# Kernel tuning notes

Measured on AMD Instinct MI355X. Metric: run time of the kernel, lower is better.

The kernel has to match this reference:

```python
import jax, jax.numpy as jnp
import numpy as np

DIM = 512
NUM_HEADS = 16
HEAD_DIM = DIM // NUM_HEADS
HIDDEN = int(DIM * 4.0)
EPS = 1e-5


def layer_norm(x, gamma, beta):
    mu = jnp.mean(x, axis=-1, keepdims=True)
    var = jnp.mean(jnp.square(x - mu), axis=-1, keepdims=True)
    return (x - mu) * jax.lax.rsqrt(var + EPS) * gamma + beta


def setup_inputs() -> dict:
    key = jax.random.key(0)
    ks = jax.random.split(key, 8)
    B, L, C = 32, 3136, DIM
    x = jax.random.normal(ks[0], (B, L, C), dtype=jnp.float32)
    norm1_g = jnp.ones((C,), jnp.float32)
    norm1_b = jnp.zeros((C,), jnp.float32)
    # spatial (per-head) mixing weight: (num_heads, head_dim, head_dim)
    w_spatial = jax.random.normal(ks[1], (NUM_HEADS, HEAD_DIM, HEAD_DIM), jnp.float32) * (1.0 / np.sqrt(HEAD_DIM))
    norm2_g = jnp.ones((C,), jnp.float32)
    norm2_b = jnp.zeros((C,), jnp.float32)
    w1 = jax.random.normal(ks[2], (C, HIDDEN), jnp.float32) * (1.0 / np.sqrt(C))
    b1 = jnp.zeros((HIDDEN,), jnp.float32)
    w2 = jax.random.normal(ks[3], (HIDDEN, C), jnp.float32) * (1.0 / np.sqrt(HIDDEN))
    b2 = jnp.zeros((C,), jnp.float32)
    return {"x": x, "norm1_g": norm1_g, "norm1_b": norm1_b, "w_spatial": w_spatial,
            "norm2_g": norm2_g, "norm2_b": norm2_b, "w1": w1, "b1": b1, "w2": w2, "b2": b2}


def reference(x, norm1_g, norm1_b, w_spatial, norm2_g, norm2_b, w1, b1, w2, b2):
    B, L, C = x.shape
    shortcut = x
    h = layer_norm(x, norm1_g, norm1_b)
    # window partition -> per-head channel-sub-dim linear (shared across windows/positions)
    # mathematically equivalent to applying the per-head matmul at every token
    h = h.reshape(B, L, NUM_HEADS, HEAD_DIM)
    h = jnp.einsum('blhd,hde->blhe', h, w_spatial)
    h = h.reshape(B, L, C)
    x = shortcut + h
    # channel MLP: Linear -> GELU(tanh) -> Linear
    y = layer_norm(x, norm2_g, norm2_b)
    y = jax.nn.gelu(y @ w1 + b1, approximate=True)
    y = y @ w2 + b2
    return x + y
```

## Files before the change

### kernel.cpp

```cpp
#include <hip/hip_runtime.h>
#include <hip/hip_bf16.h>


typedef __bf16 bf16x8 __attribute__((ext_vector_type(8)));
typedef float f32x4 __attribute__((ext_vector_type(4)));

constexpr int CDIM = 512;
constexpr int HID = 2048;
constexpr int MROWS = 32 * 3136;
constexpr float LN_EPS = 1e-5f;

static __device__ __forceinline__ float gelu_tanh(float x) {
  const float u = 0.7978845608028654f * fmaf(0.044715f * x * x, x, x);
  const float e = __expf(2.0f * u);
  return 0.5f * x * (2.0f - 2.0f / (e + 1.0f));
}

static __device__ __forceinline__ void load_lds16(const void* g, void* l) {
  __builtin_amdgcn_global_load_lds((__attribute__((address_space(1))) void*)g,
                                   (__attribute__((address_space(3))) void*)l,
                                   16, 0, 0);
}

template <int KD, int ND>
__global__ __launch_bounds__(256) void cvt_pack(const float* __restrict__ src,
                                                __hip_bfloat16* __restrict__ dst) {
  constexpr int NKT = KD / 32;
  const int o = blockIdx.x * 256 + threadIdx.x;
  const int l = o & 63;
  const int gt = o >> 6;
  const int t = gt & (NKT - 1), g = gt / NKT;
  const int n = g * 16 + (l & 15);
  const int k0 = t * 32 + (l >> 4) * 8;
  __hip_bfloat16 v[8];
#pragma unroll
  for (int j = 0; j < 8; ++j)
    v[j] = __float2bfloat16(src[(size_t)(k0 + j) * ND + n]);
  *(uint4*)(dst + (size_t)o * 8) = *(const uint4*)v;
}

__global__ __launch_bounds__(256) void fused_pre(
    const float* __restrict__ x, const float* __restrict__ g1,
    const float* __restrict__ b1, const float* __restrict__ wsp,
    const float* __restrict__ g2, const float* __restrict__ b2,
    float* __restrict__ x2out, __hip_bfloat16* __restrict__ yout) {
  __shared__ float lnbuf[2][CDIM];
  __shared__ float red[16];

  const int t = threadIdx.x;
  const int lane = t & 63;
  const int w = t >> 6;
  const int c0 = 2 * t;
  const int hd = c0 >> 5, e0 = c0 & 31;

  float wc0[32], wc1[32];
#pragma unroll
  for (int d = 0; d < 32; ++d) {
    const float2 wv = *(const float2*)&wsp[(hd * 32 + d) * 32 + e0];
    wc0[d] = wv.x;
    wc1[d] = wv.y;
  }
  const float2 g1v = *(const float2*)&g1[c0];
  const float2 b1v = *(const float2*)&b1[c0];
  const float2 g2v = *(const float2*)&g2[c0];
  const float2 b2v = *(const float2*)&b2[c0];

  for (int rp = blockIdx.x; rp < MROWS / 2; rp += gridDim.x) {
    const size_t ra = (size_t)rp * 2, rb = ra + 1;
    const float2 xa = *(const float2*)&x[ra * CDIM + c0];
    const float2 xb = *(const float2*)&x[rb * CDIM + c0];

    float sa = xa.x + xa.y, qa = xa.x * xa.x + xa.y * xa.y;
    float sb = xb.x + xb.y, qb = xb.x * xb.x + xb.y * xb.y;
#pragma unroll
    for (int off = 32; off; off >>= 1) {
      sa += __shfl_down(sa, off);
      qa += __shfl_down(qa, off);
      sb += __shfl_down(sb, off);
      qb += __shfl_down(qb, off);
    }
    if (lane == 0) {
      red[w * 4 + 0] = sa;
      red[w * 4 + 1] = qa;
      red[w * 4 + 2] = sb;
      red[w * 4 + 3] = qb;
    }
    __syncthreads();
    sa = red[0] + red[4] + red[8] + red[12];
    qa = red[1] + red[5] + red[9] + red[13];
    sb = red[2] + red[6] + red[10] + red[14];
    qb = red[3] + red[7] + red[11] + red[15];
    float mua = sa * (1.0f / CDIM), mub = sb * (1.0f / CDIM);
    float rsa = rsqrtf(qa * (1.0f / CDIM) - mua * mua + LN_EPS);
    float rsb = rsqrtf(qb * (1.0f / CDIM) - mub * mub + LN_EPS);
    lnbuf[0][c0] = (xa.x - mua) * rsa * g1v.x + b1v.x;
    lnbuf[0][c0 + 1] = (xa.y - mua) * rsa * g1v.y + b1v.y;
    lnbuf[1][c0] = (xb.x - mub) * rsb * g1v.x + b1v.x;
    lnbuf[1][c0 + 1] = (xb.y - mub) * rsb * g1v.y + b1v.y;
    __syncthreads();

    float ha0 = 0.f, ha1 = 0.f, hb0 = 0.f, hb1 = 0.f;
#pragma unroll
    for (int d = 0; d < 32; ++d) {
      const float la = lnbuf[0][hd * 32 + d];
      const float lb = lnbuf[1][hd * 32 + d];
      ha0 = fmaf(la, wc0[d], ha0);
      ha1 = fmaf(la, wc1[d], ha1);
      hb0 = fmaf(lb, wc0[d], hb0);
      hb1 = fmaf(lb, wc1[d], hb1);
    }
    const float a0 = xa.x + ha0, a1 = xa.y + ha1;
    const float b0 = xb.x + hb0, b1r = xb.y + hb1;
    float2 av;
    av.x = a0;
    av.y = a1;
    *(float2*)&x2out[ra * CDIM + c0] = av;
    av.x = b0;
    av.y = b1r;
    *(float2*)&x2out[rb * CDIM + c0] = av;

    sa = a0 + a1;
    qa = a0 * a0 + a1 * a1;
    sb = b0 + b1r;
    qb = b0 * b0 + b1r * b1r;
#pragma unroll
    for (int off = 32; off; off >>= 1) {
      sa += __shfl_down(sa, off);
      qa += __shfl_down(qa, off);
      sb += __shfl_down(sb, off);
      qb += __shfl_down(qb, off);
    }
    if (lane == 0) {
      red[w * 4 + 0] = sa;
      red[w * 4 + 1] = qa;
      red[w * 4 + 2] = sb;
      red[w * 4 + 3] = qb;
    }
    __syncthreads();
    sa = red[0] + red[4] + red[8] + red[12];
    qa = red[1] + red[5] + red[9] + red[13];
    sb = red[2] + red[6] + red[10] + red[14];
    qb = red[3] + red[7] + red[11] + red[15];
    mua = sa * (1.0f / CDIM);
    mub = sb * (1.0f / CDIM);
    rsa = rsqrtf(qa * (1.0f / CDIM) - mua * mua + LN_EPS);
    rsb = rsqrtf(qb * (1.0f / CDIM) - mub * mub + LN_EPS);
    __hip_bfloat162 yv;
    yv.x = __float2bfloat16((a0 - mua) * rsa * g2v.x + b2v.x);
    yv.y = __float2bfloat16((a1 - mua) * rsa * g2v.y + b2v.y);
    *(__hip_bfloat162*)&yout[ra * CDIM + c0] = yv;
    yv.x = __float2bfloat16((b0 - mub) * rsb * g2v.x + b2v.x);
    yv.y = __float2bfloat16((b1r - mub) * rsb * g2v.y + b2v.y);
    *(__hip_bfloat162*)&yout[rb * CDIM + c0] = yv;
    __syncthreads();
  }
}

template <int K, int N, bool GELU>
__global__ __launch_bounds__(256, 3) void gemmbs(
    const __hip_bfloat16* __restrict__ A, const char* __restrict__ Bp,
    const float* __restrict__ bias, __hip_bfloat16* __restrict__ zout,
    float* __restrict__ fout) {
  constexpr int NT = N / 128;
  constexpr int NKT = K / 32;
  __shared__ __attribute__((aligned(16))) char smem[32768];

  const int tid = threadIdx.x;
  const int lane = tid & 63;
  const int w = tid >> 6;
  const int wr = w >> 1, wc = w & 1;

  const int cpx = gridDim.x >> 3;
  const int bid = (blockIdx.x & 7) * cpx + (blockIdx.x >> 3);
  const int tm = bid / NT, tn = bid - tm * NT;
  const size_t am0 = (size_t)tm * 128;
  const int bn0 = tn * 128;

  const int r0 = tid >> 2, q0 = tid & 3;
  const __hip_bfloat16* aP0 = A + (am0 + r0) * K + q0 * 8;
  const __hip_bfloat16* aP1 = aP0 + (size_t)64 * K;
  const int wb = w * 1024;

  const int fr = lane & 15;
  const int kb = (lane >> 4) * 16;
  const int abase = (wr * 64 + fr) * 64 + kb;

  const char* bBase = Bp + ((size_t)(tn * 8 + wc * 4) * NKT) * 1024 + lane * 16;

#define STAGE_A(so, kt)                                       \
  do {                                                        \
    load_lds16(aP0 + (kt) * 32, smem + (so) + wb);            \
    load_lds16(aP1 + (kt) * 32, smem + (so) + 4096 + wb);     \
  } while (0)

  f32x4 acc[4][4] = {};
  bf16x8 bf[4], bfn[4];

  STAGE_A(0, 0);
#pragma unroll
  for (int n = 0; n < 4; ++n)
    bf[n] = *(const bf16x8*)(bBase + ((size_t)n * NKT) * 1024);
  __syncthreads();

  for (int t = 0; t < NKT; ++t) {
    const int d = (t & 1) * 8192, dn = 8192 - d;
    if (t + 1 < NKT) {
      STAGE_A(dn, t + 1);
#pragma unroll
      for (int n = 0; n < 4; ++n)
        bfn[n] = *(const bf16x8*)(bBase + ((size_t)n * NKT + t + 1) * 1024);
    }

    bf16x8 af[4];
#pragma unroll
    for (int m = 0; m < 4; ++m)
      af[m] = *(const bf16x8*)(smem + d + abase + m * 1024);
#pragma unroll
    for (int m = 0; m < 4; ++m)
#pragma unroll
      for (int n = 0; n < 4; ++n)
        acc[m][n] = __builtin_amdgcn_mfma_f32_16x16x32_bf16(af[m], bf[n],
                                                            acc[m][n], 0, 0, 0);
    if (t + 1 < NKT) {
#pragma unroll
      for (int n = 0; n < 4; ++n) bf[n] = bfn[n];
    }
    __syncthreads();
  }
#undef STAGE_A

  const int cr = (lane >> 4) * 4;
  const int cc = lane & 15;
  char* smb = smem;

  if constexpr (GELU) {
    __hip_bfloat16* ot = (__hip_bfloat16*)smb;
#pragma unroll
    for (int n = 0; n < 4; ++n) {
      const int col = wc * 64 + n * 16 + cc;
      const float bv = bias[bn0 + col];
#pragma unroll
      for (int m = 0; m < 4; ++m) {
        const int row = wr * 64 + m * 16 + cr;
#pragma unroll
        for (int j = 0; j < 4; ++j)
          ot[(row + j) * 128 + col] =
              __float2bfloat16(gelu_tanh(acc[m][n][j] + bv));
      }
    }
    __syncthreads();
#pragma unroll
    for (int it = 0; it < 8; ++it) {
      const int seg = it * 256 + tid;
      const int row = seg >> 4, cs = seg & 15;
      const uint4 v = *(const uint4*)(smb + seg * 16);
      *(uint4*)&zout[(am0 + row) * N + bn0 + cs * 8] = v;
    }
  } else {
    float* ot = (float*)smb;
#pragma unroll
    for (int p = 0; p < 2; ++p) {
      if (p) __syncthreads();
      if (wr == p) {
#pragma unroll
        for (int n = 0; n < 4; ++n) {
          const int col = wc * 64 + n * 16 + cc;
          const float bv = bias[bn0 + col];
#pragma unroll
          for (int m = 0; m < 4; ++m) {
            const int rl = m * 16 + cr;
#pragma unroll
            for (int j = 0; j < 4; ++j)
              ot[(rl + j) * 128 + col] = acc[m][n][j] + bv;
          }
        }
      }
      __syncthreads();
#pragma unroll
      for (int it = 0; it < 8; ++it) {
        const int seg = it * 256 + tid;
        const int row = seg >> 5, cs = seg & 31;
        const float4 lv = *(const float4*)(smb + seg * 16);
        float* gp = &fout[(am0 + p * 64 + row) * N + bn0 + cs * 4];
        float4 o = *(const float4*)gp;
        o.x += lv.x;
        o.y += lv.y;
        o.z += lv.z;
        o.w += lv.w;
        *(float4*)gp = o;
      }
    }
  }
}

extern "C" void kernel_launch(void* const* d_in, const int* in_sizes, int n_in,
                              void* d_out, int out_size, void* d_ws,
                              size_t ws_size, hipStream_t stream) {
  const float* x = (const float*)d_in[0];
  const float* n1g = (const float*)d_in[1];
  const float* n1b = (const float*)d_in[2];
  const float* wsp = (const float*)d_in[3];
  const float* n2g = (const float*)d_in[4];
  const float* n2b = (const float*)d_in[5];
  const float* w1 = (const float*)d_in[6];
  const float* b1 = (const float*)d_in[7];
  const float* w2 = (const float*)d_in[8];
  const float* b2 = (const float*)d_in[9];
  float* out = (float*)d_out;

  __hip_bfloat16* ybuf = (__hip_bfloat16*)d_ws;
  __hip_bfloat16* zbuf = ybuf + (size_t)MROWS * CDIM;
  __hip_bfloat16* w1p = zbuf + (size_t)MROWS * HID;
  __hip_bfloat16* w2p = w1p + (size_t)CDIM * HID;

  cvt_pack<CDIM, HID><<<512, 256, 0, stream>>>(w1, w1p);
  cvt_pack<HID, CDIM><<<512, 256, 0, stream>>>(w2, w2p);
  fused_pre<<<2048, 256, 0, stream>>>(x, n1g, n1b, wsp, n2g, n2b, out, ybuf);
  gemmbs<CDIM, HID, true><<<(MROWS / 128) * (HID / 128), 256, 0, stream>>>(
      ybuf, (const char*)w1p, b1, zbuf, nullptr);
  gemmbs<HID, CDIM, false><<<(MROWS / 128) * (CDIM / 128), 256, 0, stream>>>(
      zbuf, (const char*)w2p, b2, nullptr, out);
}
```

Before: 880.6 us.

## Switch GEMMs from 16x16x32 to 32x32x16 bf16 MFMA tiles

Replaces the 4x4 grid of 16x16x32 MFMA accumulators per warp with a 2x2 grid of 32x32x16 MFMA accumulators. The packed B-weight layout, the A fragment LDS addressing and the epilogue row/column mapping are changed to match. The larger instruction is meant to raise operand reuse per MFMA and cut LDS fragment reads. The risk is LDS bank conflicts from the new A access pattern and a different epilogue store pattern.

```diff
diff --git a/kernel.cpp b/kernel.cpp
--- a/kernel.cpp
+++ b/kernel.cpp
@@ -3,7 +3,7 @@
 
 
 typedef __bf16 bf16x8 __attribute__((ext_vector_type(8)));
-typedef float f32x4 __attribute__((ext_vector_type(4)));
+typedef float f32x16 __attribute__((ext_vector_type(16)));
 
 constexpr int CDIM = 512;
 constexpr int HID = 2048;
@@ -23,15 +23,15 @@
 }
 
 template <int KD, int ND>
-__global__ __launch_bounds__(256) void cvt_pack(const float* __restrict__ src,
-                                                __hip_bfloat16* __restrict__ dst) {
-  constexpr int NKT = KD / 32;
+__global__ __launch_bounds__(256) void cvt_pack32(
+    const float* __restrict__ src, __hip_bfloat16* __restrict__ dst) {
+  constexpr int NKT2 = KD / 16;
   const int o = blockIdx.x * 256 + threadIdx.x;
   const int l = o & 63;
   const int gt = o >> 6;
-  const int t = gt & (NKT - 1), g = gt / NKT;
-  const int n = g * 16 + (l & 15);
-  const int k0 = t * 32 + (l >> 4) * 8;
+  const int t = gt & (NKT2 - 1), g = gt / NKT2;
+  const int n = g * 32 + (l & 31);
+  const int k0 = t * 16 + (l >> 5) * 8;
   __hip_bfloat16 v[8];
 #pragma unroll
   for (int j = 0; j < 8; ++j)
@@ -157,12 +157,13 @@
 }
 
 template <int K, int N, bool GELU>
-__global__ __launch_bounds__(256, 3) void gemmbs(
+__global__ __launch_bounds__(256, 3) void gemm32(
     const __hip_bfloat16* __restrict__ A, const char* __restrict__ Bp,
     const float* __restrict__ bias, __hip_bfloat16* __restrict__ zout,
     float* __restrict__ fout) {
   constexpr int NT = N / 128;
-  constexpr int NKT = K / 32;
+  constexpr int NKT2 = K / 16;
+  constexpr int NST = K / 32;
   __shared__ __attribute__((aligned(16))) char smem[32768];
 
   const int tid = threadIdx.x;
@@ -181,11 +182,12 @@
   const __hip_bfloat16* aP1 = aP0 + (size_t)64 * K;
   const int wb = w * 1024;
 
-  const int fr = lane & 15;
-  const int kb = (lane >> 4) * 16;
-  const int abase = (wr * 64 + fr) * 64 + kb;
-
-  const char* bBase = Bp + ((size_t)(tn * 8 + wc * 4) * NKT) * 1024 + lane * 16;
+  const int arow = (lane & 31);
+  const int akb = (lane >> 5) * 16;
+  const int abase = (wr * 64 + arow) * 64 + akb;
+
+  const char* bBase =
+      Bp + ((size_t)(tn * 4 + wc * 2) * NKT2) * 1024 + lane * 16;
 
 #define STAGE_A(so, kt)                                       \
   do {                                                        \
@@ -193,60 +195,72 @@
     load_lds16(aP1 + (kt) * 32, smem + (so) + 4096 + wb);     \
   } while (0)
 
-  f32x4 acc[4][4] = {};
-  bf16x8 bf[4], bfn[4];
+  f32x16 acc[2][2] = {};
+  bf16x8 bf[2][2], bfn[2][2], af[2][2];
 
   STAGE_A(0, 0);
 #pragma unroll
-  for (int n = 0; n < 4; ++n)
-    bf[n] = *(const bf16x8*)(bBase + ((size_t)n * NKT) * 1024);
+  for (int ni = 0; ni < 2; ++ni)
+#pragma unroll
+    for (int kh = 0; kh < 2; ++kh)
+      bf[ni][kh] = *(const bf16x8*)(bBase + ((size_t)ni * NKT2 + kh) * 1024);
   __syncthreads();
 
-  for (int t = 0; t < NKT; ++t) {
+  for (int t = 0; t < NST; ++t) {
     const int d = (t & 1) * 8192, dn = 8192 - d;
-    if (t + 1 < NKT) {
+    if (t + 1 < NST) {
       STAGE_A(dn, t + 1);
 #pragma unroll
-      for (int n = 0; n < 4; ++n)
-        bfn[n] = *(const bf16x8*)(bBase + ((size_t)n * NKT + t + 1) * 1024);
-    }
-
-    bf16x8 af[4];
-#pragma unroll
-    for (int m = 0; m < 4; ++m)
-      af[m] = *(const bf16x8*)(smem + d + abase + m * 1024);
-#pragma unroll
-    for (int m = 0; m < 4; ++m)
-#pragma unroll
-      for (int n = 0; n < 4; ++n)
-        acc[m][n] = __builtin_amdgcn_mfma_f32_16x16x32_bf16(af[m], bf[n],
-                                                            acc[m][n], 0, 0, 0);
-    if (t + 1 < NKT) {
-#pragma unroll
-      for (int n = 0; n < 4; ++n) bf[n] = bfn[n];
+      for (int ni = 0; ni < 2; ++ni)
+#pragma unroll
+        for (int kh = 0; kh < 2; ++kh)
+          bfn[ni][kh] = *(const bf16x8*)(bBase +
+                                         ((size_t)ni * NKT2 + 2 * (t + 1) + kh) *
+                                             1024);
+    }
+
+#pragma unroll
+    for (int mi = 0; mi < 2; ++mi)
+#pragma unroll
+      for (int kh = 0; kh < 2; ++kh)
+        af[mi][kh] =
+            *(const bf16x8*)(smem + d + abase + mi * 2048 + kh * 32);
+#pragma unroll
+    for (int kh = 0; kh < 2; ++kh)
+#pragma unroll
+      for (int mi = 0; mi < 2; ++mi)
+#pragma unroll
+        for (int ni = 0; ni < 2; ++ni)
+          acc[mi][ni] = __builtin_amdgcn_mfma_f32_32x32x16_bf16(
+              af[mi][kh], bf[ni][kh], acc[mi][ni], 0, 0, 0);
+    if (t + 1 < NST) {
+#pragma unroll
+      for (int ni = 0; ni < 2; ++ni)
+#pragma unroll
+        for (int kh = 0; kh < 2; ++kh) bf[ni][kh] = bfn[ni][kh];
     }
     __syncthreads();
   }
 #undef STAGE_A
 
-  const int cr = (lane >> 4) * 4;
-  const int cc = lane & 15;
+  const int ccol = lane & 31;
+  const int rbase = 4 * (lane >> 5);
   char* smb = smem;
 
   if constexpr (GELU) {
     __hip_bfloat16* ot = (__hip_bfloat16*)smb;
 #pragma unroll
-    for (int n = 0; n < 4; ++n) {
-      const int col = wc * 64 + n * 16 + cc;
+    for (int ni = 0; ni < 2; ++ni) {
+      const int col = wc * 64 + ni * 32 + ccol;
       const float bv = bias[bn0 + col];
 #pragma unroll
-      for (int m = 0; m < 4; ++m) {
-        const int row = wr * 64 + m * 16 + cr;
-#pragma unroll
-        for (int j = 0; j < 4; ++j)
-          ot[(row + j) * 128 + col] =
-              __float2bfloat16(gelu_tanh(acc[m][n][j] + bv));
-      }
+      for (int mi = 0; mi < 2; ++mi)
+#pragma unroll
+        for (int r = 0; r < 16; ++r) {
+          const int row = wr * 64 + mi * 32 + (r & 3) + 8 * (r >> 2) + rbase;
+          ot[row * 128 + col] =
+              __float2bfloat16(gelu_tanh(acc[mi][ni][r] + bv));
+        }
     }
     __syncthreads();
 #pragma unroll
@@ -263,16 +277,16 @@
       if (p) __syncthreads();
       if (wr == p) {
 #pragma unroll
-        for (int n = 0; n < 4; ++n) {
-          const int col = wc * 64 + n * 16 + cc;
+        for (int ni = 0; ni < 2; ++ni) {
+          const int col = wc * 64 + ni * 32 + ccol;
           const float bv = bias[bn0 + col];
 #pragma unroll
-          for (int m = 0; m < 4; ++m) {
-            const int rl = m * 16 + cr;
-#pragma unroll
-            for (int j = 0; j < 4; ++j)
-              ot[(rl + j) * 128 + col] = acc[m][n][j] + bv;
-          }
+          for (int mi = 0; mi < 2; ++mi)
+#pragma unroll
+            for (int r = 0; r < 16; ++r) {
+              const int rl = mi * 32 + (r & 3) + 8 * (r >> 2) + rbase;
+              ot[rl * 128 + col] = acc[mi][ni][r] + bv;
+            }
         }
       }
       __syncthreads();
@@ -313,11 +327,11 @@
   __hip_bfloat16* w1p = zbuf + (size_t)MROWS * HID;
   __hip_bfloat16* w2p = w1p + (size_t)CDIM * HID;
 
-  cvt_pack<CDIM, HID><<<512, 256, 0, stream>>>(w1, w1p);
-  cvt_pack<HID, CDIM><<<512, 256, 0, stream>>>(w2, w2p);
+  cvt_pack32<CDIM, HID><<<512, 256, 0, stream>>>(w1, w1p);
+  cvt_pack32<HID, CDIM><<<512, 256, 0, stream>>>(w2, w2p);
   fused_pre<<<2048, 256, 0, stream>>>(x, n1g, n1b, wsp, n2g, n2b, out, ybuf);
-  gemmbs<CDIM, HID, true><<<(MROWS / 128) * (HID / 128), 256, 0, stream>>>(
+  gemm32<CDIM, HID, true><<<(MROWS / 128) * (HID / 128), 256, 0, stream>>>(
       ybuf, (const char*)w1p, b1, zbuf, nullptr);
-  gemmbs<HID, CDIM, false><<<(MROWS / 128) * (CDIM / 128), 256, 0, stream>>>(
+  gemm32<HID, CDIM, false><<<(MROWS / 128) * (CDIM / 128), 256, 0, stream>>>(
       zbuf, (const char*)w2p, b2, nullptr, out);
 }
```

Result: faster. 863.3 us (-2.0%).
